# Performance work log

Measured on AMD Instinct MI355X. Metric: run time of the kernel, lower is better.

## Reference

```python
import jax, jax.numpy as jnp
import numpy as np

B, V, H, W, C = 2, 4, 120, 160, 96
N_VOX = 200000
GRID = 128
VOXEL_SIZE = 0.05
DEPTH_MIN = 0.1 / VOXEL_SIZE   # 2.0 (voxel units)
DEPTH_MAX = 4.0 / VOXEL_SIZE   # 80.0 (voxel units)
STEP = 0.5                     # ray increment = voxel_size/2, in voxel units
N_STEPS = int((DEPTH_MAX - DEPTH_MIN) / STEP)  # 156


def setup_inputs() -> dict:
    key = jax.random.key(0)
    kf, kc = jax.random.split(key)
    feats = jax.random.normal(kf, (B, V, H, W, C), dtype=jnp.float32)
    # batch-sorted sparse voxel coords [N,4] = (b, x, y, z)
    xyz = jax.random.randint(kc, (N_VOX, 3), 0, GRID).astype(jnp.int32)
    bcol = jnp.repeat(jnp.arange(B, dtype=jnp.int32), N_VOX // B)[:, None]
    coords = jnp.concatenate([bcol, xyz], axis=1)
    # camera-to-world matrices in voxel units: identity rotation (looking along +z),
    # cameras at z=0 spread across x so rays sweep the grid in depth range [2, 80]
    vm = np.tile(np.eye(4, dtype=np.float32), (B, V, 1, 1))
    vm[:, :, 0, 3] = np.array([40.0, 56.0, 72.0, 88.0], dtype=np.float32)[None, :]
    vm[:, :, 1, 3] = 64.0
    vm[:, :, 2, 3] = 0.0
    view_matrix = jnp.asarray(vm)
    intrinsic_params = jnp.array([80.0, 80.0, 80.0, 60.0], dtype=jnp.float32)  # fx,fy,cx,cy
    return {"encoded_2d_features": feats, "coords": coords,
            "view_matrix": view_matrix, "intrinsic_params": intrinsic_params}


def _project(encoded_2d_features, coords, view_matrix, intrinsic_params):
    n = coords.shape[0]
    # --- per-batch coordinate shift (as in original forward) ---
    local = coords[:, 1:]
    lc = local
    local_views = view_matrix
    for b in range(B):
        m = (coords[:, 0] == b)[:, None]
        shift = jnp.min(jnp.where(m, local, jnp.iinfo(jnp.int32).max), axis=0)  # [3]
        lc = jnp.where(m, lc - shift, lc)
        local_views = local_views.at[b, :, :3, 3].add(-shift.astype(view_matrix.dtype))
    # --- dense occupancy grid, permuted to [b, z, y, x]; -1 marks empty ---
    occ = jnp.full((B, GRID, GRID, GRID), -1, dtype=jnp.int32)
    occ = occ.at[coords[:, 0], lc[:, 2], lc[:, 1], lc[:, 0]].set(
        jnp.arange(n, dtype=jnp.int32))
    # --- per-pixel ray marching ---
    fx, fy, cx, cy = intrinsic_params
    t = DEPTH_MIN + STEP * jnp.arange(N_STEPS, dtype=jnp.float32)        # [S]
    dx = (jnp.arange(W, dtype=jnp.float32) + 0.5 - cx) / fx              # [W]
    dy = (jnp.arange(H, dtype=jnp.float32) + 0.5 - cy) / fy              # [H]
    # camera-space sample points along each pixel ray: [H, W, S, 3]
    pc = jnp.stack(jnp.broadcast_arrays(
        dx[None, :, None] * t, dy[:, None, None] * t,
        jnp.broadcast_to(t, (H, W, N_STEPS))), axis=-1)
    Rm = local_views[:, :, :3, :3]   # [B,V,3,3]
    tr = local_views[:, :, :3, 3]    # [B,V,3]
    # world (grid) space points: [B, V, H, W, S, 3]
    pw = jnp.einsum('bvij,hwsj->bvhwsi', Rm, pc) + tr[:, :, None, None, None, :]
    vox = jnp.floor(pw).astype(jnp.int32)
    ix, iy, iz = vox[..., 0], vox[..., 1], vox[..., 2]
    inb = ((ix >= 0) & (ix < GRID) & (iy >= 0) & (iy < GRID) &
           (iz >= 0) & (iz < GRID))
    bidx = jnp.arange(B, dtype=jnp.int32)[:, None, None, None, None]
    occ_val = occ[bidx,
                  jnp.clip(iz, 0, GRID - 1),
                  jnp.clip(iy, 0, GRID - 1),
                  jnp.clip(ix, 0, GRID - 1)]
    vox_id = jnp.where(inb, occ_val, -1)                                  # [B,V,H,W,S]
    # first occupied voxel hit along each ray
    hit = vox_id >= 0
    first = jnp.argmax(hit, axis=-1)                                      # [B,V,H,W]
    has_hit = jnp.any(hit, axis=-1)
    hit_id = jnp.take_along_axis(vox_id, first[..., None], axis=-1)[..., 0]
    tgt = jnp.where(has_hit, hit_id, n).reshape(-1)   # index n = dump slot for misses
    # scatter-accumulate pixel features into voxel slots + per-voxel counts
    flat_feat = encoded_2d_features.reshape(-1, C)
    proj = jnp.zeros((n + 1, C), dtype=encoded_2d_features.dtype).at[tgt].add(flat_feat)[:n]
    cnt = jnp.zeros((n + 1,), dtype=jnp.int32).at[tgt].add(1)[:n]
    out = proj / (cnt[:, None].astype(proj.dtype) + 1e-4)
    return out, cnt


def reference(encoded_2d_features, coords, view_matrix, intrinsic_params):
    return _project(encoded_2d_features, coords, view_matrix, intrinsic_params)
```

## Files before the change

### kernel.cpp

```cpp
#include <hip/hip_runtime.h>
#include <hip/hip_bf16.h>
#include <climits>

#define B_ 2
#define V_ 4
#define H_ 120
#define W_ 160
#define C_ 96
#define NVOX 200000
#define GRID_ 128
#define NSTEPS 156
#define NRAYS (B_*V_*H_*W_)
#define NB1 ((NVOX + 255) / 256)
#define CHUNK 32
#define OUTQ2 ((NVOX * C_) / 4)
#define NTHREADS_OCC (NB1 * 256)
#define NTHREADS_MARCH (2400 * 256)


__global__ void occ_kernel(const int* __restrict__ coords,
                           int* __restrict__ occ,
                           unsigned long long* __restrict__ mask,
                           float* __restrict__ out) {
    int i = blockIdx.x * blockDim.x + threadIdx.x;
    if (i < NVOX) {
        int b = coords[i * 4 + 0];
        int x = coords[i * 4 + 1];
        int y = coords[i * 4 + 2];
        int z = coords[i * 4 + 3];
        int idx = ((b * GRID_ + z) * GRID_ + y) * GRID_ + x;
        atomicMax(&occ[idx], i);
        atomicOr(&mask[idx >> 6], 1ull << (idx & 63));
    }
    float4 z4 = make_float4(0.f, 0.f, 0.f, 0.f);
    float4* o4 = (float4*)out;
    for (int q = blockIdx.x * blockDim.x + threadIdx.x; q < OUTQ2; q += NTHREADS_OCC)
        o4[q] = z4;
}

__global__ void march_kernel(const float* __restrict__ vm,
                             const float* __restrict__ intr,
                             const unsigned long long* __restrict__ mask,
                             const int* __restrict__ occ,
                             int* __restrict__ tgt,
                             int* __restrict__ cnt) {
    int gt   = blockIdx.x * blockDim.x + threadIdx.x;
    int lane = threadIdx.x & 63;
    int p    = lane & 15;
    int sub  = lane >> 4;
    int r    = ((gt >> 6) << 4) + p;
    int w = r % W_;
    int h = (r / W_) % H_;
    int v = (r / (W_ * H_)) % V_;
    int b = r / (W_ * H_ * V_);
    const float* M = vm + (size_t)(b * V_ + v) * 16;
    float fx = intr[0], fy = intr[1], cx = intr[2], cy = intr[3];
    float dx = ((float)w + 0.5f - cx) / fx;
    float dy = ((float)h + 0.5f - cy) / fy;
    float d0 = M[0] * dx + M[1] * dy + M[2];
    float d1 = M[4] * dx + M[5] * dy + M[6];
    float d2 = M[8] * dx + M[9] * dy + M[10];
    float t0 = M[3];
    float t1 = M[7];
    float t2 = M[11];
    const int vbase = b * GRID_ * GRID_ * GRID_;
    const int MISS = 0x7FFFFFFF;
    int beststep = MISS;
    for (int w0 = 0; w0 < NSTEPS; w0 += 32) {
        int lin[8]; bool ok[8];
#pragma unroll
        for (int j = 0; j < 8; ++j) {
            int st = w0 + sub * 8 + j;
            float t = 2.0f + 0.5f * (float)st;
            float pwx = d0 * t + t0;
            float pwy = d1 * t + t1;
            float pwz = d2 * t + t2;
            int ix = (int)floorf(pwx);
            int iy = (int)floorf(pwy);
            int iz = (int)floorf(pwz);
            ok[j] = ((unsigned)ix < (unsigned)GRID_) &
                    ((unsigned)iy < (unsigned)GRID_) &
                    ((unsigned)iz < (unsigned)GRID_) & (st < NSTEPS);
            int cix = min(max(ix, 0), GRID_ - 1);
            int ciy = min(max(iy, 0), GRID_ - 1);
            int ciz = min(max(iz, 0), GRID_ - 1);
            lin[j] = vbase + (ciz << 14) + (ciy << 7) + cix;
        }
        unsigned long long u[8];
        bool same[8];
        same[0] = false;
#pragma unroll
        for (int j = 1; j < 8; ++j) same[j] = ((lin[j] >> 6) == (lin[j - 1] >> 6));
#pragma unroll
        for (int j = 0; j < 8; ++j)
            if (!same[j]) u[j] = mask[lin[j] >> 6];
#pragma unroll
        for (int j = 1; j < 8; ++j)
            if (same[j]) u[j] = u[j - 1];
        int local = MISS;
#pragma unroll
        for (int j = 0; j < 8; ++j) {
            int st = w0 + sub * 8 + j;
            if (ok[j] && ((u[j] >> (lin[j] & 63)) & 1ull)) local = min(local, st);
        }
        local = min(local, __shfl_xor(local, 16));
        local = min(local, __shfl_xor(local, 32));
        if (local != MISS) { beststep = local; break; }
    }
    int res = -1;
    if (sub == 0) {
        if (beststep != MISS) {
            float t = 2.0f + 0.5f * (float)beststep;
            int ix = (int)floorf(d0 * t + t0);
            int iy = (int)floorf(d1 * t + t1);
            int iz = (int)floorf(d2 * t + t2);
            res = occ[vbase + (iz << 14) + (iy << 7) + ix];
        }
        tgt[r] = res;
    }
    bool active = (sub == 0) && (res >= 0);
    int prevres = __shfl_up(res, 1);
    bool head = active && (p == 0 || prevres != res);
    bool boundary = head || !active;
    unsigned long long bb = __ballot(boundary);
    if (head) {
        unsigned long long above = bb & ~((2ull << lane) - 1);
        int next = above ? (__ffsll((long long)above) - 1) : 64;
        atomicAdd(&cnt[res], next - lane);
    }
}

__device__ __forceinline__ void flush_run(int t, float ax, float ay, int lane,
                                          const int* __restrict__ cnt,
                                          float* __restrict__ out) {
    float denom = (float)cnt[t] + 0.0001f;
    if (lane < 48) {
        unsafeAtomicAdd(out + (size_t)t * C_ + 2 * lane,     ax / denom);
        unsafeAtomicAdd(out + (size_t)t * C_ + 2 * lane + 1, ay / denom);
    }
}

__global__ void scatter_kernel(const float* __restrict__ feats,
                               const int* __restrict__ tgt,
                               const int* __restrict__ cnt,
                               float* __restrict__ out,
                               float* __restrict__ cnt_out) {
    int gthread = blockIdx.x * blockDim.x + threadIdx.x;
    int lane = threadIdx.x & 63;
    if (gthread < NVOX) cnt_out[gthread] = (float)cnt[gthread];
    int wave = gthread >> 6;
    int a = wave * CHUNK;
    int myt = (lane < CHUNK) ? tgt[a + lane] : -1;
    float ax = 0.0f, ay = 0.0f;
    int cur = -1;
    for (int k0 = 0; k0 < CHUNK; k0 += 8) {
        float2 vbuf[8]; int tt[8];
#pragma unroll
        for (int j = 0; j < 8; ++j) {
            int k = k0 + j;
            tt[j] = __shfl(myt, k);
            vbuf[j] = make_float2(0.0f, 0.0f);
            if (tt[j] >= 0 && lane < 48)
                vbuf[j] = ((const float2*)(feats + (size_t)(a + k) * C_))[lane];
        }
#pragma unroll
        for (int j = 0; j < 8; ++j) {
            if (tt[j] != cur) {
                if (cur >= 0) flush_run(cur, ax, ay, lane, cnt, out);
                cur = tt[j]; ax = 0.0f; ay = 0.0f;
            }
            ax += vbuf[j].x; ay += vbuf[j].y;
        }
    }
    if (cur >= 0) flush_run(cur, ax, ay, lane, cnt, out);
}

extern "C" void kernel_launch(void* const* d_in, const int* in_sizes, int n_in,
                              void* d_out, int out_size, void* d_ws, size_t ws_size,
                              hipStream_t stream) {
    const float* feats  = (const float*)d_in[0];
    const int*   coords = (const int*)d_in[1];
    const float* vm     = (const float*)d_in[2];
    const float* intr   = (const float*)d_in[3];

    float* out     = (float*)d_out;
    float* cnt_out = out + (size_t)NVOX * C_;

    char* ws = (char*)d_ws;
    int*                cnt  = (int*)(ws + 64);
    unsigned long long* mask = (unsigned long long*)(ws + 800064);
    int*  tgt = (int*)(ws + 1324416);
    int*  occ = (int*)(ws + 4786816);

    (void)hipMemsetAsync(ws, 0, 1324352, stream);

    occ_kernel<<<NB1, 256, 0, stream>>>(coords, occ, mask, out);
    march_kernel<<<2400, 256, 0, stream>>>(vm, intr, mask, occ, tgt, cnt);
    scatter_kernel<<<NRAYS / CHUNK / 4, 256, 0, stream>>>(feats, tgt, cnt, out, cnt_out);
}
```

Baseline: 192.4 us.

## Clip ray march to grid AABB and move output zeroing into march

Each ray now computes its slab intersection with the 128^3 grid box. The step range is reduced across the wavefront with shuffles, so the march loop only visits 32-step windows that can be inside the grid. This skips mask lookups for steps that are out of bounds. The zero-fill of the output buffer moves from the occupancy kernel into the march kernel, so that memory traffic overlaps with the march's latency-bound loads. The scatter kernel doubles its per-wave chunk to 64 rays and uses a strided loop to write counts. The risks are division by a zero direction component (relying on inf semantics) and a heavier march kernel.

```diff
diff --git a/kernel.cpp b/kernel.cpp
--- a/kernel.cpp
+++ b/kernel.cpp
@@ -12,30 +12,23 @@
 #define NSTEPS 156
 #define NRAYS (B_*V_*H_*W_)
 #define NB1 ((NVOX + 255) / 256)
-#define CHUNK 32
+#define CHUNK 64
 #define OUTQ2 ((NVOX * C_) / 4)
-#define NTHREADS_OCC (NB1 * 256)
 #define NTHREADS_MARCH (2400 * 256)
 
 
 __global__ void occ_kernel(const int* __restrict__ coords,
                            int* __restrict__ occ,
-                           unsigned long long* __restrict__ mask,
-                           float* __restrict__ out) {
+                           unsigned long long* __restrict__ mask) {
     int i = blockIdx.x * blockDim.x + threadIdx.x;
-    if (i < NVOX) {
-        int b = coords[i * 4 + 0];
-        int x = coords[i * 4 + 1];
-        int y = coords[i * 4 + 2];
-        int z = coords[i * 4 + 3];
-        int idx = ((b * GRID_ + z) * GRID_ + y) * GRID_ + x;
-        atomicMax(&occ[idx], i);
-        atomicOr(&mask[idx >> 6], 1ull << (idx & 63));
-    }
-    float4 z4 = make_float4(0.f, 0.f, 0.f, 0.f);
-    float4* o4 = (float4*)out;
-    for (int q = blockIdx.x * blockDim.x + threadIdx.x; q < OUTQ2; q += NTHREADS_OCC)
-        o4[q] = z4;
+    if (i >= NVOX) return;
+    int b = coords[i * 4 + 0];
+    int x = coords[i * 4 + 1];
+    int y = coords[i * 4 + 2];
+    int z = coords[i * 4 + 3];
+    int idx = ((b * GRID_ + z) * GRID_ + y) * GRID_ + x;
+    atomicMax(&occ[idx], i);
+    atomicOr(&mask[idx >> 6], 1ull << (idx & 63));
 }
 
 __global__ void march_kernel(const float* __restrict__ vm,
@@ -43,91 +36,114 @@
                              const unsigned long long* __restrict__ mask,
                              const int* __restrict__ occ,
                              int* __restrict__ tgt,
-                             int* __restrict__ cnt) {
+                             int* __restrict__ cnt,
+                             float* __restrict__ out) {
     int gt   = blockIdx.x * blockDim.x + threadIdx.x;
     int lane = threadIdx.x & 63;
     int p    = lane & 15;
     int sub  = lane >> 4;
     int r    = ((gt >> 6) << 4) + p;
-    int w = r % W_;
-    int h = (r / W_) % H_;
-    int v = (r / (W_ * H_)) % V_;
-    int b = r / (W_ * H_ * V_);
-    const float* M = vm + (size_t)(b * V_ + v) * 16;
-    float fx = intr[0], fy = intr[1], cx = intr[2], cy = intr[3];
-    float dx = ((float)w + 0.5f - cx) / fx;
-    float dy = ((float)h + 0.5f - cy) / fy;
-    float d0 = M[0] * dx + M[1] * dy + M[2];
-    float d1 = M[4] * dx + M[5] * dy + M[6];
-    float d2 = M[8] * dx + M[9] * dy + M[10];
-    float t0 = M[3];
-    float t1 = M[7];
-    float t2 = M[11];
-    const int vbase = b * GRID_ * GRID_ * GRID_;
-    const int MISS = 0x7FFFFFFF;
-    int beststep = MISS;
-    for (int w0 = 0; w0 < NSTEPS; w0 += 32) {
-        int lin[8]; bool ok[8];
-#pragma unroll
-        for (int j = 0; j < 8; ++j) {
-            int st = w0 + sub * 8 + j;
-            float t = 2.0f + 0.5f * (float)st;
-            float pwx = d0 * t + t0;
-            float pwy = d1 * t + t1;
-            float pwz = d2 * t + t2;
-            int ix = (int)floorf(pwx);
-            int iy = (int)floorf(pwy);
-            int iz = (int)floorf(pwz);
-            ok[j] = ((unsigned)ix < (unsigned)GRID_) &
-                    ((unsigned)iy < (unsigned)GRID_) &
-                    ((unsigned)iz < (unsigned)GRID_) & (st < NSTEPS);
-            int cix = min(max(ix, 0), GRID_ - 1);
-            int ciy = min(max(iy, 0), GRID_ - 1);
-            int ciz = min(max(iz, 0), GRID_ - 1);
-            lin[j] = vbase + (ciz << 14) + (ciy << 7) + cix;
-        }
-        unsigned long long u[8];
-        bool same[8];
-        same[0] = false;
-#pragma unroll
-        for (int j = 1; j < 8; ++j) same[j] = ((lin[j] >> 6) == (lin[j - 1] >> 6));
-#pragma unroll
-        for (int j = 0; j < 8; ++j)
-            if (!same[j]) u[j] = mask[lin[j] >> 6];
-#pragma unroll
-        for (int j = 1; j < 8; ++j)
-            if (same[j]) u[j] = u[j - 1];
-        int local = MISS;
-#pragma unroll
-        for (int j = 0; j < 8; ++j) {
-            int st = w0 + sub * 8 + j;
-            if (ok[j] && ((u[j] >> (lin[j] & 63)) & 1ull)) local = min(local, st);
-        }
-        local = min(local, __shfl_xor(local, 16));
-        local = min(local, __shfl_xor(local, 32));
-        if (local != MISS) { beststep = local; break; }
+    {
+        int w = r % W_;
+        int h = (r / W_) % H_;
+        int v = (r / (W_ * H_)) % V_;
+        int b = r / (W_ * H_ * V_);
+        const float* M = vm + (size_t)(b * V_ + v) * 16;
+        float fx = intr[0], fy = intr[1], cx = intr[2], cy = intr[3];
+        float dx = ((float)w + 0.5f - cx) / fx;
+        float dy = ((float)h + 0.5f - cy) / fy;
+        float d0 = M[0] * dx + M[1] * dy + M[2];
+        float d1 = M[4] * dx + M[5] * dy + M[6];
+        float d2 = M[8] * dx + M[9] * dy + M[10];
+        float t0 = M[3];
+        float t1 = M[7];
+        float t2 = M[11];
+        float i0 = 1.0f / d0, i1 = 1.0f / d1, i2 = 1.0f / d2;
+        float a0 = (0.0f - t0) * i0, b0 = (128.0f - t0) * i0;
+        float a1 = (0.0f - t1) * i1, b1 = (128.0f - t1) * i1;
+        float a2 = (0.0f - t2) * i2, b2 = (128.0f - t2) * i2;
+        float tlo = fmaxf(fmaxf(fminf(a0, b0), fminf(a1, b1)), fminf(a2, b2));
+        float thi = fminf(fminf(fmaxf(a0, b0), fmaxf(a1, b1)), fmaxf(a2, b2));
+        bool dead = !(tlo <= thi);
+        float slo = fmaxf((tlo - 2.0f) * 2.0f, 0.0f);
+        float shi = fminf((thi - 2.0f) * 2.0f, (float)(NSTEPS - 1));
+        int st_lo = dead ? NSTEPS : max(0, (int)slo - 1);
+        int st_hi = dead ? -1 : min(NSTEPS - 1, (int)shi + 1);
+        int wlo = st_lo, whi = st_hi;
+#pragma unroll
+        for (int m = 1; m < 64; m <<= 1) {
+            wlo = min(wlo, __shfl_xor(wlo, m));
+            whi = max(whi, __shfl_xor(whi, m));
+        }
+        const int vbase = b * GRID_ * GRID_ * GRID_;
+        const int MISS = 0x7FFFFFFF;
+        int beststep = MISS;
+        for (int w0 = (wlo & ~31); w0 <= whi; w0 += 32) {
+            int lin[8]; bool ok[8];
+#pragma unroll
+            for (int j = 0; j < 8; ++j) {
+                int st = w0 + sub * 8 + j;
+                float t = 2.0f + 0.5f * (float)st;
+                float pwx = d0 * t + t0;
+                float pwy = d1 * t + t1;
+                float pwz = d2 * t + t2;
+                int ix = (int)floorf(pwx);
+                int iy = (int)floorf(pwy);
+                int iz = (int)floorf(pwz);
+                ok[j] = ((unsigned)ix < (unsigned)GRID_) &
+                        ((unsigned)iy < (unsigned)GRID_) &
+                        ((unsigned)iz < (unsigned)GRID_) & (st < NSTEPS);
+                int cix = min(max(ix, 0), GRID_ - 1);
+                int ciy = min(max(iy, 0), GRID_ - 1);
+                int ciz = min(max(iz, 0), GRID_ - 1);
+                lin[j] = vbase + (ciz << 14) + (ciy << 7) + cix;
+            }
+            unsigned long long u[8];
+            bool same[8];
+            same[0] = false;
+#pragma unroll
+            for (int j = 1; j < 8; ++j) same[j] = ((lin[j] >> 6) == (lin[j - 1] >> 6));
+#pragma unroll
+            for (int j = 0; j < 8; ++j)
+                if (!same[j]) u[j] = mask[lin[j] >> 6];
+#pragma unroll
+            for (int j = 1; j < 8; ++j)
+                if (same[j]) u[j] = u[j - 1];
+            int local = MISS;
+#pragma unroll
+            for (int j = 0; j < 8; ++j) {
+                int st = w0 + sub * 8 + j;
+                if (ok[j] && ((u[j] >> (lin[j] & 63)) & 1ull)) local = min(local, st);
+            }
+            local = min(local, __shfl_xor(local, 16));
+            local = min(local, __shfl_xor(local, 32));
+            if (local != MISS) { beststep = local; break; }
+        }
+        int res = -1;
+        if (sub == 0) {
+            if (beststep != MISS) {
+                float t = 2.0f + 0.5f * (float)beststep;
+                int ix = (int)floorf(d0 * t + t0);
+                int iy = (int)floorf(d1 * t + t1);
+                int iz = (int)floorf(d2 * t + t2);
+                res = occ[vbase + (iz << 14) + (iy << 7) + ix];
+            }
+            tgt[r] = res;
+        }
+        bool active = (sub == 0) && (res >= 0);
+        int prevres = __shfl_up(res, 1);
+        bool head = active && (p == 0 || prevres != res);
+        bool boundary = head || !active;
+        unsigned long long bb = __ballot(boundary);
+        if (head) {
+            unsigned long long above = bb & ~((2ull << lane) - 1);
+            int next = above ? (__ffsll((long long)above) - 1) : 64;
+            atomicAdd(&cnt[res], next - lane);
+        }
     }
-    int res = -1;
-    if (sub == 0) {
-        if (beststep != MISS) {
-            float t = 2.0f + 0.5f * (float)beststep;
-            int ix = (int)floorf(d0 * t + t0);
-            int iy = (int)floorf(d1 * t + t1);
-            int iz = (int)floorf(d2 * t + t2);
-            res = occ[vbase + (iz << 14) + (iy << 7) + ix];
-        }
-        tgt[r] = res;
-    }
-    bool active = (sub == 0) && (res >= 0);
-    int prevres = __shfl_up(res, 1);
-    bool head = active && (p == 0 || prevres != res);
-    bool boundary = head || !active;
-    unsigned long long bb = __ballot(boundary);
-    if (head) {
-        unsigned long long above = bb & ~((2ull << lane) - 1);
-        int next = above ? (__ffsll((long long)above) - 1) : 64;
-        atomicAdd(&cnt[res], next - lane);
-    }
+    float4 z4 = make_float4(0.f, 0.f, 0.f, 0.f);
+    float4* o4 = (float4*)out;
+    for (int i = gt; i < OUTQ2; i += NTHREADS_MARCH) o4[i] = z4;
 }
 
 __device__ __forceinline__ void flush_run(int t, float ax, float ay, int lane,
@@ -147,10 +163,11 @@
                                float* __restrict__ cnt_out) {
     int gthread = blockIdx.x * blockDim.x + threadIdx.x;
     int lane = threadIdx.x & 63;
-    if (gthread < NVOX) cnt_out[gthread] = (float)cnt[gthread];
+    for (int i = gthread; i < NVOX; i += NRAYS)
+        cnt_out[i] = (float)cnt[i];
     int wave = gthread >> 6;
     int a = wave * CHUNK;
-    int myt = (lane < CHUNK) ? tgt[a + lane] : -1;
+    int myt = tgt[a + lane];
     float ax = 0.0f, ay = 0.0f;
     int cur = -1;
     for (int k0 = 0; k0 < CHUNK; k0 += 8) {
@@ -194,7 +211,7 @@
 
     (void)hipMemsetAsync(ws, 0, 1324352, stream);
 
-    occ_kernel<<<NB1, 256, 0, stream>>>(coords, occ, mask, out);
-    march_kernel<<<2400, 256, 0, stream>>>(vm, intr, mask, occ, tgt, cnt);
-    scatter_kernel<<<NRAYS / CHUNK / 4, 256, 0, stream>>>(feats, tgt, cnt, out, cnt_out);
-}
+    occ_kernel<<<NB1, 256, 0, stream>>>(coords, occ, mask);
+    march_kernel<<<2400, 256, 0, stream>>>(vm, intr, mask, occ, tgt, cnt, out);
+    scatter_kernel<<<NRAYS / 256, 256, 0, stream>>>(feats, tgt, cnt, out, cnt_out);
+}
```

Measured after the change: 189.6 us. About the same (-1.4%).

## Software-pipeline march mask loads, move output zeroing, halve scatter chunk

Applied to the files above, without the earlier changes.

The ray-march loop is unrolled into a double-buffered schedule: the mask words for the next 32-step window are loaded before the current window is evaluated, hiding global load latency. The per-step 'same word' dedup is dropped, so every step issues a load. Zeroing of the output buffer moves from occ_kernel to the end of march_kernel, which puts it on the longer kernel and shortens occ_kernel. The scatter chunk drops to 16 rays per wave with all loads issued up front, which doubles the number of waves and so the parallelism for loading features.

```diff
diff --git a/kernel.cpp b/kernel.cpp
--- a/kernel.cpp
+++ b/kernel.cpp
@@ -12,122 +12,129 @@
 #define NSTEPS 156
 #define NRAYS (B_*V_*H_*W_)
 #define NB1 ((NVOX + 255) / 256)
-#define CHUNK 32
+#define CHUNK 16
 #define OUTQ2 ((NVOX * C_) / 4)
-#define NTHREADS_OCC (NB1 * 256)
 #define NTHREADS_MARCH (2400 * 256)
 
 
 __global__ void occ_kernel(const int* __restrict__ coords,
                            int* __restrict__ occ,
-                           unsigned long long* __restrict__ mask,
-                           float* __restrict__ out) {
+                           unsigned long long* __restrict__ mask) {
     int i = blockIdx.x * blockDim.x + threadIdx.x;
-    if (i < NVOX) {
-        int b = coords[i * 4 + 0];
-        int x = coords[i * 4 + 1];
-        int y = coords[i * 4 + 2];
-        int z = coords[i * 4 + 3];
-        int idx = ((b * GRID_ + z) * GRID_ + y) * GRID_ + x;
-        atomicMax(&occ[idx], i);
-        atomicOr(&mask[idx >> 6], 1ull << (idx & 63));
-    }
-    float4 z4 = make_float4(0.f, 0.f, 0.f, 0.f);
-    float4* o4 = (float4*)out;
-    for (int q = blockIdx.x * blockDim.x + threadIdx.x; q < OUTQ2; q += NTHREADS_OCC)
-        o4[q] = z4;
-}
+    if (i >= NVOX) return;
+    int b = coords[i * 4 + 0];
+    int x = coords[i * 4 + 1];
+    int y = coords[i * 4 + 2];
+    int z = coords[i * 4 + 3];
+    int idx = ((b * GRID_ + z) * GRID_ + y) * GRID_ + x;
+    atomicMax(&occ[idx], i);
+    atomicOr(&mask[idx >> 6], 1ull << (idx & 63));
+}
+
+#define MARCH_COMPUTE(LIN, OK, W0)                                          \
+    _Pragma("unroll")                                                       \
+    for (int j = 0; j < 8; ++j) {                                           \
+        int st = (W0) + sub * 8 + j;                                        \
+        float t = 2.0f + 0.5f * (float)st;                                  \
+        int ix = (int)floorf(d0 * t + t0);                                  \
+        int iy = (int)floorf(d1 * t + t1);                                  \
+        int iz = (int)floorf(d2 * t + t2);                                  \
+        OK[j] = ((unsigned)ix < (unsigned)GRID_) &                          \
+                ((unsigned)iy < (unsigned)GRID_) &                          \
+                ((unsigned)iz < (unsigned)GRID_) & (st < NSTEPS);           \
+        int cix = min(max(ix, 0), GRID_ - 1);                               \
+        int ciy = min(max(iy, 0), GRID_ - 1);                               \
+        int ciz = min(max(iz, 0), GRID_ - 1);                               \
+        LIN[j] = vbase + (ciz << 14) + (ciy << 7) + cix;                    \
+    }
+
+#define MARCH_LOAD(U, LIN)                                                  \
+    _Pragma("unroll")                                                       \
+    for (int j = 0; j < 8; ++j) U[j] = mask[LIN[j] >> 6];
+
+#define MARCH_EVAL(U, LIN, OK, W0)                                          \
+    {                                                                       \
+        int local = MISS;                                                   \
+        _Pragma("unroll")                                                   \
+        for (int j = 0; j < 8; ++j) {                                       \
+            int st = (W0) + sub * 8 + j;                                    \
+            if (OK[j] && ((U[j] >> (LIN[j] & 63)) & 1ull))                  \
+                local = min(local, st);                                     \
+        }                                                                   \
+        local = min(local, __shfl_xor(local, 16));                          \
+        local = min(local, __shfl_xor(local, 32));                          \
+        if (local != MISS) { beststep = local; goto resolved; }             \
+    }
 
 __global__ void march_kernel(const float* __restrict__ vm,
                              const float* __restrict__ intr,
                              const unsigned long long* __restrict__ mask,
                              const int* __restrict__ occ,
                              int* __restrict__ tgt,
-                             int* __restrict__ cnt) {
+                             int* __restrict__ cnt,
+                             float* __restrict__ out) {
     int gt   = blockIdx.x * blockDim.x + threadIdx.x;
     int lane = threadIdx.x & 63;
     int p    = lane & 15;
     int sub  = lane >> 4;
     int r    = ((gt >> 6) << 4) + p;
-    int w = r % W_;
-    int h = (r / W_) % H_;
-    int v = (r / (W_ * H_)) % V_;
-    int b = r / (W_ * H_ * V_);
-    const float* M = vm + (size_t)(b * V_ + v) * 16;
-    float fx = intr[0], fy = intr[1], cx = intr[2], cy = intr[3];
-    float dx = ((float)w + 0.5f - cx) / fx;
-    float dy = ((float)h + 0.5f - cy) / fy;
-    float d0 = M[0] * dx + M[1] * dy + M[2];
-    float d1 = M[4] * dx + M[5] * dy + M[6];
-    float d2 = M[8] * dx + M[9] * dy + M[10];
-    float t0 = M[3];
-    float t1 = M[7];
-    float t2 = M[11];
-    const int vbase = b * GRID_ * GRID_ * GRID_;
-    const int MISS = 0x7FFFFFFF;
-    int beststep = MISS;
-    for (int w0 = 0; w0 < NSTEPS; w0 += 32) {
-        int lin[8]; bool ok[8];
-#pragma unroll
-        for (int j = 0; j < 8; ++j) {
-            int st = w0 + sub * 8 + j;
-            float t = 2.0f + 0.5f * (float)st;
-            float pwx = d0 * t + t0;
-            float pwy = d1 * t + t1;
-            float pwz = d2 * t + t2;
-            int ix = (int)floorf(pwx);
-            int iy = (int)floorf(pwy);
-            int iz = (int)floorf(pwz);
-            ok[j] = ((unsigned)ix < (unsigned)GRID_) &
-                    ((unsigned)iy < (unsigned)GRID_) &
-                    ((unsigned)iz < (unsigned)GRID_) & (st < NSTEPS);
-            int cix = min(max(ix, 0), GRID_ - 1);
-            int ciy = min(max(iy, 0), GRID_ - 1);
-            int ciz = min(max(iz, 0), GRID_ - 1);
-            lin[j] = vbase + (ciz << 14) + (ciy << 7) + cix;
+    {
+        int w = r % W_;
+        int h = (r / W_) % H_;
+        int v = (r / (W_ * H_)) % V_;
+        int b = r / (W_ * H_ * V_);
+        const float* M = vm + (size_t)(b * V_ + v) * 16;
+        float fx = intr[0], fy = intr[1], cx = intr[2], cy = intr[3];
+        float dx = ((float)w + 0.5f - cx) / fx;
+        float dy = ((float)h + 0.5f - cy) / fy;
+        float d0 = M[0] * dx + M[1] * dy + M[2];
+        float d1 = M[4] * dx + M[5] * dy + M[6];
+        float d2 = M[8] * dx + M[9] * dy + M[10];
+        float t0 = M[3];
+        float t1 = M[7];
+        float t2 = M[11];
+        const int vbase = b * GRID_ * GRID_ * GRID_;
+        const int MISS = 0x7FFFFFFF;
+        int beststep = MISS;
+        int res = -1;
+        int linA[8], linB[8];
+        bool okA[8], okB[8];
+        unsigned long long uA[8], uB[8];
+        MARCH_COMPUTE(linA, okA, 0)   MARCH_LOAD(uA, linA)
+        MARCH_COMPUTE(linB, okB, 32)  MARCH_LOAD(uB, linB)
+        MARCH_EVAL(uA, linA, okA, 0)
+        MARCH_COMPUTE(linA, okA, 64)  MARCH_LOAD(uA, linA)
+        MARCH_EVAL(uB, linB, okB, 32)
+        MARCH_COMPUTE(linB, okB, 96)  MARCH_LOAD(uB, linB)
+        MARCH_EVAL(uA, linA, okA, 64)
+        MARCH_COMPUTE(linA, okA, 128) MARCH_LOAD(uA, linA)
+        MARCH_EVAL(uB, linB, okB, 96)
+        MARCH_EVAL(uA, linA, okA, 128)
+resolved:
+        if (sub == 0) {
+            if (beststep != MISS) {
+                float t = 2.0f + 0.5f * (float)beststep;
+                int ix = (int)floorf(d0 * t + t0);
+                int iy = (int)floorf(d1 * t + t1);
+                int iz = (int)floorf(d2 * t + t2);
+                res = occ[vbase + (iz << 14) + (iy << 7) + ix];
+            }
+            tgt[r] = res;
         }
-        unsigned long long u[8];
-        bool same[8];
-        same[0] = false;
-#pragma unroll
-        for (int j = 1; j < 8; ++j) same[j] = ((lin[j] >> 6) == (lin[j - 1] >> 6));
-#pragma unroll
-        for (int j = 0; j < 8; ++j)
-            if (!same[j]) u[j] = mask[lin[j] >> 6];
-#pragma unroll
-        for (int j = 1; j < 8; ++j)
-            if (same[j]) u[j] = u[j - 1];
-        int local = MISS;
-#pragma unroll
-        for (int j = 0; j < 8; ++j) {
-            int st = w0 + sub * 8 + j;
-            if (ok[j] && ((u[j] >> (lin[j] & 63)) & 1ull)) local = min(local, st);
+        bool active = (sub == 0) && (res >= 0);
+        int prevres = __shfl_up(res, 1);
+        bool head = active && (p == 0 || prevres != res);
+        bool boundary = head || !active;
+        unsigned long long bb = __ballot(boundary);
+        if (head) {
+            unsigned long long above = bb & ~((2ull << lane) - 1);
+            int next = above ? (__ffsll((long long)above) - 1) : 64;
+            atomicAdd(&cnt[res], next - lane);
         }
-        local = min(local, __shfl_xor(local, 16));
-        local = min(local, __shfl_xor(local, 32));
-        if (local != MISS) { beststep = local; break; }
-    }
-    int res = -1;
-    if (sub == 0) {
-        if (beststep != MISS) {
-            float t = 2.0f + 0.5f * (float)beststep;
-            int ix = (int)floorf(d0 * t + t0);
-            int iy = (int)floorf(d1 * t + t1);
-            int iz = (int)floorf(d2 * t + t2);
-            res = occ[vbase + (iz << 14) + (iy << 7) + ix];
-        }
-        tgt[r] = res;
-    }
-    bool active = (sub == 0) && (res >= 0);
-    int prevres = __shfl_up(res, 1);
-    bool head = active && (p == 0 || prevres != res);
-    bool boundary = head || !active;
-    unsigned long long bb = __ballot(boundary);
-    if (head) {
-        unsigned long long above = bb & ~((2ull << lane) - 1);
-        int next = above ? (__ffsll((long long)above) - 1) : 64;
-        atomicAdd(&cnt[res], next - lane);
-    }
+    }
+    float4 z4 = make_float4(0.f, 0.f, 0.f, 0.f);
+    float4* o4 = (float4*)out;
+    for (int i = gt; i < OUTQ2; i += NTHREADS_MARCH) o4[i] = z4;
 }
 
 __device__ __forceinline__ void flush_run(int t, float ax, float ay, int lane,
@@ -151,26 +158,23 @@
     int wave = gthread >> 6;
     int a = wave * CHUNK;
     int myt = (lane < CHUNK) ? tgt[a + lane] : -1;
+    float2 vbuf[CHUNK]; int tt[CHUNK];
+#pragma unroll
+    for (int k = 0; k < CHUNK; ++k) {
+        tt[k] = __shfl(myt, k);
+        vbuf[k] = make_float2(0.0f, 0.0f);
+        if (tt[k] >= 0 && lane < 48)
+            vbuf[k] = ((const float2*)(feats + (size_t)(a + k) * C_))[lane];
+    }
     float ax = 0.0f, ay = 0.0f;
     int cur = -1;
-    for (int k0 = 0; k0 < CHUNK; k0 += 8) {
-        float2 vbuf[8]; int tt[8];
 #pragma unroll
-        for (int j = 0; j < 8; ++j) {
-            int k = k0 + j;
-            tt[j] = __shfl(myt, k);
-            vbuf[j] = make_float2(0.0f, 0.0f);
-            if (tt[j] >= 0 && lane < 48)
-                vbuf[j] = ((const float2*)(feats + (size_t)(a + k) * C_))[lane];
+    for (int k = 0; k < CHUNK; ++k) {
+        if (tt[k] != cur) {
+            if (cur >= 0) flush_run(cur, ax, ay, lane, cnt, out);
+            cur = tt[k]; ax = 0.0f; ay = 0.0f;
         }
-#pragma unroll
-        for (int j = 0; j < 8; ++j) {
-            if (tt[j] != cur) {
-                if (cur >= 0) flush_run(cur, ax, ay, lane, cnt, out);
-                cur = tt[j]; ax = 0.0f; ay = 0.0f;
-            }
-            ax += vbuf[j].x; ay += vbuf[j].y;
-        }
+        ax += vbuf[k].x; ay += vbuf[k].y;
     }
     if (cur >= 0) flush_run(cur, ax, ay, lane, cnt, out);
 }
@@ -194,7 +198,7 @@
 
     (void)hipMemsetAsync(ws, 0, 1324352, stream);
 
-    occ_kernel<<<NB1, 256, 0, stream>>>(coords, occ, mask, out);
-    march_kernel<<<2400, 256, 0, stream>>>(vm, intr, mask, occ, tgt, cnt);
-    scatter_kernel<<<NRAYS / CHUNK / 4, 256, 0, stream>>>(feats, tgt, cnt, out, cnt_out);
-}
+    occ_kernel<<<NB1, 256, 0, stream>>>(coords, occ, mask);
+    march_kernel<<<2400, 256, 0, stream>>>(vm, intr, mask, occ, tgt, cnt, out);
+    scatter_kernel<<<NRAYS * 4 / 256, 256, 0, stream>>>(feats, tgt, cnt, out, cnt_out);
+}
```

Result: slower. 201.5 us (+4.7%).
